# Performance work log

Hardware: AMD Instinct MI355X
Metric: run time of the kernel (lower is better)

Reference implementation:

```python
import jax, jax.numpy as jnp
import numpy as np

N0 = 50000
N1 = 50000
E = 500000
IN_DIM = 128
OUT_DIM = 128
H = 8
DK = OUT_DIM // H  # 16
SQRT_DK = float(np.sqrt(DK))
NUM_TYPES = 2
NUM_REL = 3
# relations: (src_type, dst_type, e_id)
RELATIONS = [(0, 1, 0), (1, 0, 1), (0, 0, 2)]


def setup_inputs() -> dict:
    key = jax.random.key(0)
    ks = jax.random.split(key, 24)
    d = {}
    d["h0"] = jax.random.normal(ks[0], (N0, IN_DIM), dtype=jnp.float32)
    d["h1"] = jax.random.normal(ks[1], (N1, IN_DIM), dtype=jnp.float32)
    d["src0"] = jax.random.randint(ks[2], (E,), 0, N0)
    d["dst0"] = jax.random.randint(ks[3], (E,), 0, N1)
    d["src1"] = jax.random.randint(ks[4], (E,), 0, N1)
    d["dst1"] = jax.random.randint(ks[5], (E,), 0, N0)
    d["src2"] = jax.random.randint(ks[6], (E,), 0, N0)
    d["dst2"] = jax.random.randint(ks[7], (E,), 0, N0)
    w_scale = 1.0 / np.sqrt(IN_DIM)
    # per-node-type stacked linear weights (k, q, v, a), torch Linear convention: y = x @ W.T + b
    d["Wk"] = jax.random.normal(ks[8], (NUM_TYPES, OUT_DIM, IN_DIM), dtype=jnp.float32) * w_scale
    d["bk"] = jnp.zeros((NUM_TYPES, OUT_DIM), dtype=jnp.float32)
    d["Wq"] = jax.random.normal(ks[9], (NUM_TYPES, OUT_DIM, IN_DIM), dtype=jnp.float32) * w_scale
    d["bq"] = jnp.zeros((NUM_TYPES, OUT_DIM), dtype=jnp.float32)
    d["Wv"] = jax.random.normal(ks[10], (NUM_TYPES, OUT_DIM, IN_DIM), dtype=jnp.float32) * w_scale
    d["bv"] = jnp.zeros((NUM_TYPES, OUT_DIM), dtype=jnp.float32)
    d["Wa"] = jax.random.normal(ks[11], (NUM_TYPES, OUT_DIM, OUT_DIM), dtype=jnp.float32) * w_scale
    d["ba"] = jnp.zeros((NUM_TYPES, OUT_DIM), dtype=jnp.float32)
    xavier = float(np.sqrt(6.0 / (DK + DK)))
    d["rel_att"] = jax.random.uniform(ks[12], (NUM_REL, H, DK, DK), dtype=jnp.float32, minval=-xavier, maxval=xavier)
    d["rel_msg"] = jax.random.uniform(ks[13], (NUM_REL, H, DK, DK), dtype=jnp.float32, minval=-xavier, maxval=xavier)
    d["rel_pri"] = jnp.ones((NUM_REL, H), dtype=jnp.float32)
    d["skip"] = jnp.ones((NUM_TYPES,), dtype=jnp.float32)
    return d


def _lin(x, W, b):
    return x @ W.T + b


def reference(h0, h1, src0, dst0, src1, dst1, src2, dst2,
              Wk, bk, Wq, bq, Wv, bv, Wa, ba,
              rel_att, rel_msg, rel_pri, skip):
    h = [h0, h1]
    edges = [(src0, dst0), (src1, dst1), (src2, dst2)]
    # per-type projections, reshaped to (N, H, DK)
    k = [_lin(h[t], Wk[t], bk[t]).reshape(-1, H, DK) for t in range(NUM_TYPES)]
    q = [_lin(h[t], Wq[t], bq[t]).reshape(-1, H, DK) for t in range(NUM_TYPES)]
    v = [_lin(h[t], Wv[t], bv[t]).reshape(-1, H, DK) for t in range(NUM_TYPES)]

    agg = [[] for _ in range(NUM_TYPES)]
    for (s, dt, e), (src, dst) in zip(RELATIONS, edges):
        # relation-specific transforms of source k and v
        kr = jnp.einsum('nhi,hij->nhj', k[s], rel_att[e])
        vr = jnp.einsum('nhi,hij->nhj', v[s], rel_msg[e])
        # per-edge dot-product score (E, H)
        score = (q[dt][dst] * kr[src]).sum(-1) * rel_pri[e] / SQRT_DK
        n_dst = h[dt].shape[0]
        # edge softmax normalized by dst (stable)
        m = jax.ops.segment_max(score, dst, num_segments=n_dst)
        ex = jnp.exp(score - m[dst])
        den = jax.ops.segment_sum(ex, dst, num_segments=n_dst)
        attn = ex / den[dst]  # (E, H)
        # weighted message scatter-sum -> (n_dst, H, DK)
        msg = vr[src] * attn[:, :, None]
        agg[dt].append(jax.ops.segment_sum(msg, dst, num_segments=n_dst))

    new_h = []
    for t in range(NUM_TYPES):
        # cross_reducer='mean' over relations targeting this node type
        tmean = sum(agg[t]) / float(len(agg[t]))
        tflat = tmean.reshape(-1, OUT_DIM)
        trans = _lin(tflat, Wa[t], ba[t])  # dropout = identity (eval)
        alpha = jax.nn.sigmoid(skip[t])
        new_h.append(trans * alpha + h[t] * (1.0 - alpha))
    return tuple(new_h)
```

## Files before the change

### kernel.cpp

```cpp
#include <hip/hip_runtime.h>

typedef __attribute__((ext_vector_type(8))) short bf16x8;
typedef __attribute__((ext_vector_type(4))) float f32x4;

#define NB 196
#define CHK 2048
#define CAPB 4096

__device__ __forceinline__ float bflo(unsigned u) { return __uint_as_float(u << 16); }
__device__ __forceinline__ float bfhi(unsigned u) { return __uint_as_float(u & 0xFFFF0000u); }
__device__ __forceinline__ unsigned f2bf(float f) {
  unsigned u = __float_as_uint(f);
  u = (u + 0x7FFFu + ((u >> 16) & 1u)) >> 16;
  return u;
}

__global__ void cvt2_kernel(const float* __restrict__ a, unsigned short* __restrict__ oa,
                            const float* __restrict__ b, unsigned short* __restrict__ ob,
                            int n8) {
  int i = blockIdx.x * 256 + threadIdx.x;
  if (i >= n8) return;
  const float* in = blockIdx.y ? b : a;
  unsigned short* out = blockIdx.y ? ob : oa;
  const float4* p = (const float4*)(in + (size_t)i * 8);
  float4 x = p[0], y = p[1];
  uint4 v;
  v.x = f2bf(x.x) | (f2bf(x.y) << 16);
  v.y = f2bf(x.z) | (f2bf(x.w) << 16);
  v.z = f2bf(y.x) | (f2bf(y.y) << 16);
  v.w = f2bf(y.z) | (f2bf(y.w) << 16);
  *(uint4*)(out + (size_t)i * 8) = v;
}

__global__ void compose_w_kernel(const float* __restrict__ Wk, const float* __restrict__ bk,
                                 const float* __restrict__ Wv, const float* __restrict__ bv,
                                 const float* __restrict__ rel_att, const float* __restrict__ rel_msg,
                                 const float* __restrict__ rel_pri,
                                 unsigned short* __restrict__ Wkr, float* __restrict__ bkr,
                                 unsigned short* __restrict__ Wvr, float* __restrict__ bvr) {
  int e = blockIdx.x;
  int o = blockIdx.y;
  int z = blockIdx.z;
  int c = threadIdx.x;
  int hd = o >> 4, j = o & 15;
  const int se[3] = {0, 1, 0};
  int s = se[e];
  const float* W = z ? Wv : Wk;
  const float* b = z ? bv : bk;
  const float* R = z ? rel_msg : rel_att;
  float scale = z ? 1.0f : (rel_pri[e * 8 + hd] * 0.25f);
  float acc = 0.0f, bacc = 0.0f;
#pragma unroll
  for (int i = 0; i < 16; ++i) {
    float r = R[((e * 8 + hd) * 16 + i) * 16 + j];
    acc += W[(s * 128 + hd * 16 + i) * 128 + c] * r;
    bacc += b[s * 128 + hd * 16 + i] * r;
  }
  unsigned short* Wo = z ? Wvr : Wkr;
  float* bo = z ? bvr : bkr;
  Wo[((size_t)e * 128 + o) * 128 + c] = (unsigned short)f2bf(acc * scale);
  if (c == 0) bo[e * 128 + o] = bacc * scale;
}

struct ProjFP {
  const float* A[2];
  int M[2];
  int nj[2];
  const unsigned short* W[10];
  const float* b[10];
  unsigned short* out[10];
  int ostr[10];
};

__global__ __launch_bounds__(256) void proj_gemm_fused(ProjFP P) {
  __shared__ short As[128 * 128];
  __shared__ short Bs[128 * 128];
  int type = blockIdx.y;
  const float* __restrict__ A = P.A[type];
  int M = P.M[type];
  int nj = P.nj[type];
  int base = type * 5;
  int row0 = blockIdx.x * 128;
  if (row0 >= M) return;
  int t = threadIdx.x;
  bool full = (row0 + 128 <= M);
#pragma unroll
  for (int it = 0; it < 8; ++it) {
    int o = (it * 256 + t) * 8;
    int row = o >> 7, col = o & 127;
    int gr = row0 + row;
    uint4 av = make_uint4(0, 0, 0, 0);
    if (full || gr < M) {
      float4 x = *(const float4*)(A + (size_t)gr * 128 + col);
      float4 y = *(const float4*)(A + (size_t)gr * 128 + col + 4);
      av.x = f2bf(x.x) | (f2bf(x.y) << 16);
      av.y = f2bf(x.z) | (f2bf(x.w) << 16);
      av.z = f2bf(y.x) | (f2bf(y.y) << 16);
      av.w = f2bf(y.z) | (f2bf(y.w) << 16);
    }
    int sw = o ^ ((row & 7) << 3);
    *(uint4*)(&As[sw]) = av;
  }
  {
    const unsigned short* W0 = P.W[base];
#pragma unroll
    for (int it = 0; it < 8; ++it) {
      int o = (it * 256 + t) * 8;
      int row = o >> 7;
      int sw = o ^ ((row & 7) << 3);
      *(uint4*)(&Bs[sw]) = *(const uint4*)(W0 + o);
    }
  }
  __syncthreads();
  int wid = t >> 6, l = t & 63;
  int wr = wid >> 1, wc = wid & 1;
  int lr = l & 15, kb = l >> 4;
  for (int j = 0;; ++j) {
    f32x4 acc[4][4] = {};
#pragma unroll
    for (int ks = 0; ks < 4; ++ks) {
      bf16x8 af[4], bfr[4];
#pragma unroll
      for (int m = 0; m < 4; ++m) {
        int row = wr * 64 + m * 16 + lr;
        int h = (row * 128 + kb * 8 + ks * 32) ^ ((row & 7) << 3);
        af[m] = *(bf16x8*)(&As[h]);
      }
#pragma unroll
      for (int n = 0; n < 4; ++n) {
        int row = wc * 64 + n * 16 + lr;
        int h = (row * 128 + kb * 8 + ks * 32) ^ ((row & 7) << 3);
        bfr[n] = *(bf16x8*)(&Bs[h]);
      }
#pragma unroll
      for (int m = 0; m < 4; ++m)
#pragma unroll
        for (int n = 0; n < 4; ++n)
          acc[m][n] = __builtin_amdgcn_mfma_f32_16x16x32_bf16(af[m], bfr[n], acc[m][n], 0, 0, 0);
    }
    const float* bias = P.b[base + j];
    unsigned short* out = P.out[base + j];
    int ostr = P.ostr[base + j];
    int rb = row0 + wr * 64 + (l >> 4) * 4;
#pragma unroll
    for (int m = 0; m < 4; ++m)
#pragma unroll
      for (int jr = 0; jr < 4; ++jr) {
        int grow = rb + m * 16 + jr;
        if (grow < M) {
#pragma unroll
          for (int n = 0; n < 4; ++n) {
            int col = wc * 64 + n * 16 + lr;
            out[(size_t)grow * ostr + col] = (unsigned short)f2bf(acc[m][n][jr] + bias[col]);
          }
        }
      }
    if (j + 1 >= nj) break;
    __syncthreads();
    {
      const unsigned short* Wj = P.W[base + j + 1];
#pragma unroll
      for (int it = 0; it < 8; ++it) {
        int o = (it * 256 + t) * 8;
        int row = o >> 7;
        int sw = o ^ ((row & 7) << 3);
        *(uint4*)(&Bs[sw]) = *(const uint4*)(Wj + o);
      }
    }
    __syncthreads();
  }
}

__global__ __launch_bounds__(256) void final_gemm_mfma(
    float* __restrict__ dout, const unsigned short* __restrict__ Tb0,
    const unsigned short* __restrict__ Tb1, const unsigned short* __restrict__ Wab,
    const float* __restrict__ ba, const float* __restrict__ h0, const float* __restrict__ h1,
    const float* __restrict__ skip, int N0, int N1) {
  __shared__ short As[128 * 128];
  __shared__ short Bs[128 * 128];
  int type = blockIdx.y;
  int M = type ? N1 : N0;
  const unsigned short* T = type ? Tb1 : Tb0;
  const unsigned short* W = Wab + (size_t)type * 16384;
  const float* bias = ba + type * 128;
  const float* h = type ? h1 : h0;
  float* O = dout + (type ? (size_t)N0 * 128 : 0);
  int row0 = blockIdx.x * 128;
  if (row0 >= M) return;
  int t = threadIdx.x;
  bool full = (row0 + 128 <= M);
#pragma unroll
  for (int it = 0; it < 8; ++it) {
    int o = (it * 256 + t) * 8;
    int row = o >> 7;
    int gr = row0 + row;
    uint4 av = make_uint4(0, 0, 0, 0);
    if (full || gr < M) av = *(const uint4*)(T + (size_t)gr * 128 + (o & 127));
    int sw = o ^ ((row & 7) << 3);
    *(uint4*)(&As[sw]) = av;
    uint4 wv = *(const uint4*)(W + o);
    *(uint4*)(&Bs[sw]) = wv;
  }
  __syncthreads();
  int wid = t >> 6, l = t & 63;
  int wr = wid >> 1, wc = wid & 1;
  int lr = l & 15, kb = l >> 4;
  f32x4 acc[4][4] = {};
#pragma unroll
  for (int ks = 0; ks < 4; ++ks) {
    bf16x8 af[4], bfr[4];
#pragma unroll
    for (int m = 0; m < 4; ++m) {
      int row = wr * 64 + m * 16 + lr;
      int h2 = (row * 128 + kb * 8 + ks * 32) ^ ((row & 7) << 3);
      af[m] = *(bf16x8*)(&As[h2]);
    }
#pragma unroll
    for (int n = 0; n < 4; ++n) {
      int row = wc * 64 + n * 16 + lr;
      int h2 = (row * 128 + kb * 8 + ks * 32) ^ ((row & 7) << 3);
      bfr[n] = *(bf16x8*)(&Bs[h2]);
    }
#pragma unroll
    for (int m = 0; m < 4; ++m)
#pragma unroll
      for (int n = 0; n < 4; ++n)
        acc[m][n] = __builtin_amdgcn_mfma_f32_16x16x32_bf16(af[m], bfr[n], acc[m][n], 0, 0, 0);
  }
  float alpha = 1.0f / (1.0f + __expf(-skip[type]));
  float beta = 1.0f - alpha;
  int rb = row0 + wr * 64 + (l >> 4) * 4;
#pragma unroll
  for (int m = 0; m < 4; ++m)
#pragma unroll
    for (int jr = 0; jr < 4; ++jr) {
      int grow = rb + m * 16 + jr;
      if (grow < M) {
#pragma unroll
        for (int n = 0; n < 4; ++n) {
          int col = wc * 64 + n * 16 + lr;
          float vout = alpha * (acc[m][n][jr] + bias[col]) + beta * h[(size_t)grow * 128 + col];
          O[(size_t)grow * 128 + col] = vout;
        }
      }
    }
}


__global__ __launch_bounds__(256) void bhist_kernel(const int* __restrict__ d0,
                                                    const int* __restrict__ d1,
                                                    const int* __restrict__ d2,
                                                    int* __restrict__ bh, int E) {
  __shared__ int lh[NB];
  int r = blockIdx.y;
  const int* dst = r == 0 ? d0 : (r == 1 ? d1 : d2);
  int t = threadIdx.x;
  int lo = blockIdx.x * CHK;
  int hi = lo + CHK < E ? lo + CHK : E;
  for (int j = t; j < NB; j += 256) lh[j] = 0;
  __syncthreads();
  for (int i = lo + t; i < hi; i += 256) atomicAdd(&lh[dst[i] >> 8], 1);
  __syncthreads();
  for (int j = t; j < NB; j += 256) {
    int v = lh[j];
    if (v) atomicAdd(&bh[r * NB + j], v);
  }
}

__global__ void bscan_kernel(const int* __restrict__ bh, int* __restrict__ bbase, int E) {
  __shared__ int sdm[256];
  int r = blockIdx.x;
  int t = threadIdx.x;
  int v = (t < NB) ? bh[r * NB + t] : 0;
  sdm[t] = v;
  __syncthreads();
  for (int off = 1; off < 256; off <<= 1) {
    int u = (t >= off) ? sdm[t - off] : 0;
    __syncthreads();
    sdm[t] += u;
    __syncthreads();
  }
  if (t < NB) bbase[r * (NB + 1) + t] = sdm[t] - v;
  if (t == 0) bbase[r * (NB + 1) + NB] = E;
}

__global__ __launch_bounds__(256) void bin_kernel(
    const int* __restrict__ s0, const int* __restrict__ d0, const int* __restrict__ s1,
    const int* __restrict__ d1, const int* __restrict__ s2, const int* __restrict__ d2,
    const int* __restrict__ bbase, int* __restrict__ bcur, int2* __restrict__ bo0,
    int2* __restrict__ bo1, int2* __restrict__ bo2, int E) {
  __shared__ int2 st[CHK];
  __shared__ int ga[CHK];
  __shared__ int hist[NB];
  __shared__ int scn[256];
  __shared__ int gb[NB];
  int r = blockIdx.y;
  const int* src = r == 0 ? s0 : (r == 1 ? s1 : s2);
  const int* dst = r == 0 ? d0 : (r == 1 ? d1 : d2);
  int2* bo = r == 0 ? bo0 : (r == 1 ? bo1 : bo2);
  const int* bb = bbase + r * (NB + 1);
  int t = threadIdx.x;
  int lo = blockIdx.x * CHK;
  int hi = lo + CHK < E ? lo + CHK : E;
  int nloc = hi - lo;
  if (nloc <= 0) return;
  for (int j = t; j < NB; j += 256) hist[j] = 0;
  __syncthreads();
  int myb[CHK / 256], myr[CHK / 256];
  int2 mye[CHK / 256];
#pragma unroll
  for (int k = 0; k < CHK / 256; ++k) {
    int i = lo + k * 256 + t;
    myb[k] = -1;
    if (i < hi) {
      int d = dst[i];
      int b = d >> 8;
      mye[k] = make_int2(src[i], d);
      myb[k] = b;
      myr[k] = atomicAdd(&hist[b], 1);
    }
  }
  __syncthreads();
  int v = (t < NB) ? hist[t] : 0;
  scn[t] = v;
  __syncthreads();
  for (int off = 1; off < 256; off <<= 1) {
    int u = (t >= off) ? scn[t - off] : 0;
    __syncthreads();
    scn[t] += u;
    __syncthreads();
  }
  int excl = scn[t] - v;
  __syncthreads();
  scn[t] = excl;
  if (t < NB && v > 0) gb[t] = atomicAdd(&bcur[r * NB + t], v);
  __syncthreads();
#pragma unroll
  for (int k = 0; k < CHK / 256; ++k) {
    if (myb[k] >= 0) {
      int slot = scn[myb[k]] + myr[k];
      st[slot] = mye[k];
      ga[slot] = bb[myb[k]] + gb[myb[k]] + myr[k];
    }
  }
  __syncthreads();
  for (int j = t; j < nloc; j += 256) bo[ga[j]] = st[j];
}

__global__ __launch_bounds__(256) void bsort_kernel(
    const int2* __restrict__ bo0, const int2* __restrict__ bo1, const int2* __restrict__ bo2,
    const int* __restrict__ bbase, int* __restrict__ rp0, int* __restrict__ rp1,
    int* __restrict__ rp2, int* __restrict__ ss0, int* __restrict__ ss1, int* __restrict__ ss2,
    int* __restrict__ dof0, int* __restrict__ dof1, int* __restrict__ dof2, int nd0, int nd1,
    int nd2, int E) {
  __shared__ int2 ed[CAPB];
  __shared__ int ssrt[CAPB];
  __shared__ unsigned short rank[CAPB];
  __shared__ unsigned short dsrtu[CAPB];
  __shared__ int hist[256];
  __shared__ int scn[256];
  int r = blockIdx.y, b = blockIdx.x;
  const int2* bo = r == 0 ? bo0 : (r == 1 ? bo1 : bo2);
  int* rp = r == 0 ? rp0 : (r == 1 ? rp1 : rp2);
  int* ss = r == 0 ? ss0 : (r == 1 ? ss1 : ss2);
  int* dof = r == 0 ? dof0 : (r == 1 ? dof1 : dof2);
  int nd = r == 0 ? nd0 : (r == 1 ? nd1 : nd2);
  const int* bb = bbase + r * (NB + 1);
  int base = bb[b], endb = bb[b + 1];
  int cnt = endb - base;
  if (cnt > CAPB) cnt = CAPB;
  int nlo = b << 8;
  int nn = nd - nlo;
  if (nn > 256) nn = 256;
  int t = threadIdx.x;
  hist[t] = 0;
  for (int j = t; j < cnt; j += 256) ed[j] = bo[base + j];
  __syncthreads();
  for (int j = t; j < cnt; j += 256) {
    int node = ed[j].y & 255;
    rank[j] = (unsigned short)atomicAdd(&hist[node], 1);
  }
  __syncthreads();
  int v = hist[t];
  scn[t] = v;
  __syncthreads();
  for (int off = 1; off < 256; off <<= 1) {
    int u = (t >= off) ? scn[t - off] : 0;
    __syncthreads();
    scn[t] += u;
    __syncthreads();
  }
  int excl = scn[t] - v;
  __syncthreads();
  scn[t] = excl;
  __syncthreads();
  if (t < nn) rp[nlo + t] = base + excl;
  if (b == 0 && t == 0) rp[nd] = E;
  for (int j = t; j < cnt; j += 256) {
    int node = ed[j].y & 255;
    int slot = scn[node] + rank[j];
    ssrt[slot] = ed[j].x;
    dsrtu[slot] = (unsigned short)node;
  }
  __syncthreads();
  for (int j = t; j < cnt; j += 256) {
    ss[base + j] = ssrt[j];
    dof[base + j] = nlo + dsrtu[j];
  }
}

struct ScP {
  const int* ss[3];
  const int* dof[3];
  const unsigned* kv[3];
  const unsigned* qb[3];
  unsigned short* eb[3];
  int E;
};

__global__ __launch_bounds__(256) void score_kernel(ScP P) {
  int r = blockIdx.y;
  const int* __restrict__ ss = P.ss[r];
  const int* __restrict__ dof = P.dof[r];
  const unsigned* __restrict__ kv = P.kv[r];
  const unsigned* __restrict__ qb = P.qb[r];
  unsigned short* __restrict__ eb = P.eb[r];
  int t = threadIdx.x;
  int p = blockIdx.x * 32 + (t >> 3);
  if (p >= P.E) return;
  int h = t & 7;
  int s = ss[p];
  int d = dof[p];
  const uint4* kr = (const uint4*)((const char*)kv + ((size_t)(unsigned)s << 9) + h * 32);
  const uint4* qr = (const uint4*)((const char*)qb + ((size_t)(unsigned)d << 8) + h * 32);
  uint4 k1 = kr[0], k2 = kr[1];
  uint4 q1 = qr[0], q2 = qr[1];
  float sc = 0.f;
#pragma unroll
  for (int c = 0; c < 4; ++c) {
    unsigned ku = ((const unsigned*)&k1)[c], qu = ((const unsigned*)&q1)[c];
    sc = fmaf(bflo(ku), bflo(qu), sc);
    sc = fmaf(bfhi(ku), bfhi(qu), sc);
  }
#pragma unroll
  for (int c = 0; c < 4; ++c) {
    unsigned ku = ((const unsigned*)&k2)[c], qu = ((const unsigned*)&q2)[c];
    sc = fmaf(bflo(ku), bflo(qu), sc);
    sc = fmaf(bfhi(ku), bfhi(qu), sc);
  }
  eb[(size_t)p * 8 + h] = (unsigned short)f2bf(__expf(sc));
}

struct AgP {
  const int *ss0, *ss1, *ss2;
  const unsigned short *eb0, *eb1, *eb2;
  const unsigned *kv0, *kv1, *kv2;
  const int *rp0, *rp1, *rp2;
  unsigned *Tb0, *Tb1;
  int N0, N1;
};

__device__ __forceinline__ void agg_rel(const int* __restrict__ ss,
                                        const unsigned short* __restrict__ eb,
                                        const unsigned* __restrict__ kv,
                                        const int* __restrict__ rp, int node, int l,
                                        float& r0, float& r1) {
  int beg = __builtin_amdgcn_readfirstlane(rp[node]);
  int end = __builtin_amdgcn_readfirstlane(rp[node + 1]);
  if (end <= beg) return;
  int h = l >> 3;
  const char* kvl = (const char*)kv + 256 + l * 4;
  float a0 = 0.f, a1 = 0.f, den = 0.f;
  for (int p = beg; p < end; p += 4) {
    int idx = p + (l & 3);
    idx = idx < end ? idx : end - 1;
    int sv = ss[idx];
#pragma unroll
    for (int j = 0; j < 4; ++j) {
      int pj = p + j;
      bool valid = pj < end;
      int pj2 = valid ? pj : end - 1;
      int s = __builtin_amdgcn_readlane(sv, j);
      float e = __uint_as_float((unsigned)eb[(size_t)pj2 * 8 + h] << 16);
      if (j && !valid) e = 0.f;
      unsigned v = *(const unsigned*)(kvl + ((size_t)(unsigned)s << 9));
      den += e;
      a0 = fmaf(e, bflo(v), a0);
      a1 = fmaf(e, bfhi(v), a1);
    }
  }
  float inv = 1.0f / den;
  r0 = fmaf(a0, inv, r0);
  r1 = fmaf(a1, inv, r1);
}

__global__ __launch_bounds__(256) void agg2_kernel(AgP P) {
  int gw = (blockIdx.x * 256 + threadIdx.x) >> 6;
  int l = threadIdx.x & 63;
  if (gw < P.N0) {
    float r0 = 0.f, r1 = 0.f;
    agg_rel(P.ss1, P.eb1, P.kv1, P.rp1, gw, l, r0, r1);
    agg_rel(P.ss2, P.eb2, P.kv2, P.rp2, gw, l, r0, r1);
    P.Tb0[(size_t)gw * 64 + l] = f2bf(r0 * 0.5f) | (f2bf(r1 * 0.5f) << 16);
  } else if (gw < P.N0 + P.N1) {
    int n = gw - P.N0;
    float r0 = 0.f, r1 = 0.f;
    agg_rel(P.ss0, P.eb0, P.kv0, P.rp0, n, l, r0, r1);
    P.Tb1[(size_t)n * 64 + l] = f2bf(r0) | (f2bf(r1) << 16);
  }
}

extern "C" void kernel_launch(void* const* d_in, const int* in_sizes, int n_in,
                              void* d_out, int out_size, void* d_ws, size_t ws_size,
                              hipStream_t stream) {
  const float* h0 = (const float*)d_in[0];
  const float* h1 = (const float*)d_in[1];
  const int* srcs[3] = {(const int*)d_in[2], (const int*)d_in[4], (const int*)d_in[6]};
  const int* dsts[3] = {(const int*)d_in[3], (const int*)d_in[5], (const int*)d_in[7]};
  const float* Wk = (const float*)d_in[8];
  const float* bk = (const float*)d_in[9];
  const float* Wq = (const float*)d_in[10];
  const float* bq = (const float*)d_in[11];
  const float* Wv = (const float*)d_in[12];
  const float* bv = (const float*)d_in[13];
  const float* Wa = (const float*)d_in[14];
  const float* ba = (const float*)d_in[15];
  const float* rel_att = (const float*)d_in[16];
  const float* rel_msg = (const float*)d_in[17];
  const float* rel_pri = (const float*)d_in[18];
  const float* skip = (const float*)d_in[19];

  int N0 = in_sizes[0] / 128;
  int N1 = in_sizes[1] / 128;
  int E = in_sizes[2];
  int nsrc[3] = {N0, N1, N0};
  int ndst[3] = {N1, N0, N0};
  int maxN = N0 > N1 ? N0 : N1;

  char* base = (char*)d_ws;
  size_t off = 0;
  auto alloc = [&](size_t bytes) -> void* {
    void* p = base + off;
    off += (bytes + 255) & ~(size_t)255;
    return p;
  };

  unsigned short* qb0 = (unsigned short*)alloc((size_t)N0 * 128 * 2);
  unsigned short* qb1 = (unsigned short*)alloc((size_t)N1 * 128 * 2);
  unsigned short* kvb[3];
  for (int r = 0; r < 3; ++r) kvb[r] = (unsigned short*)alloc((size_t)nsrc[r] * 256 * 2);
  unsigned short* Tb0 = (unsigned short*)alloc((size_t)N0 * 128 * 2);
  unsigned short* Tb1 = (unsigned short*)alloc((size_t)N1 * 128 * 2);
  unsigned short* Wkrb = (unsigned short*)alloc((size_t)3 * 16384 * 2);
  unsigned short* Wvrb = (unsigned short*)alloc((size_t)3 * 16384 * 2);
  unsigned short* Wqb = (unsigned short*)alloc((size_t)2 * 16384 * 2);
  unsigned short* Wab = (unsigned short*)alloc((size_t)2 * 16384 * 2);
  float* bkr = (float*)alloc(3 * 128 * 4);
  float* bvr = (float*)alloc(3 * 128 * 4);
  int* rp[3];
  int* ssb[3];
  int* dof[3];
  unsigned short* eb[3];
  int2* bo[3];
  for (int r = 0; r < 3; ++r) {
    rp[r] = (int*)alloc((size_t)(ndst[r] + 1) * 4);
    ssb[r] = (int*)alloc((size_t)(E + 8) * 4);
    dof[r] = (int*)alloc((size_t)(E + 8) * 4);
    eb[r] = (unsigned short*)alloc((size_t)E * 8 * 2);
    bo[r] = (int2*)alloc((size_t)(E + 8) * 8);
  }
  int* bcnt = (int*)alloc((size_t)2 * 3 * NB * 4);
  int* bhist = bcnt;
  int* bcur = bcnt + 3 * NB;
  int* bbase = (int*)alloc((size_t)3 * (NB + 1) * 4);
  (void)ws_size;

  compose_w_kernel<<<dim3(3, 128, 2), 128, 0, stream>>>(Wk, bk, Wv, bv, rel_att, rel_msg,
                                                        rel_pri, Wkrb, bkr, Wvrb, bvr);
  cvt2_kernel<<<dim3(16, 2), 256, 0, stream>>>(Wq, Wqb, Wa, Wab, 4096);

  ProjFP pf;
  pf.A[0] = h0; pf.A[1] = h1;
  pf.M[0] = N0; pf.M[1] = N1;
  pf.nj[0] = 5; pf.nj[1] = 3;
  pf.W[0] = Wqb;            pf.b[0] = bq;        pf.out[0] = qb0;          pf.ostr[0] = 128;
  pf.W[1] = Wkrb;           pf.b[1] = bkr;       pf.out[1] = kvb[0];       pf.ostr[1] = 256;
  pf.W[2] = Wkrb + 32768;   pf.b[2] = bkr + 256; pf.out[2] = kvb[2];       pf.ostr[2] = 256;
  pf.W[3] = Wvrb;           pf.b[3] = bvr;       pf.out[3] = kvb[0] + 128; pf.ostr[3] = 256;
  pf.W[4] = Wvrb + 32768;   pf.b[4] = bvr + 256; pf.out[4] = kvb[2] + 128; pf.ostr[4] = 256;
  pf.W[5] = Wqb + 16384;    pf.b[5] = bq + 128;  pf.out[5] = qb1;          pf.ostr[5] = 128;
  pf.W[6] = Wkrb + 16384;   pf.b[6] = bkr + 128; pf.out[6] = kvb[1];       pf.ostr[6] = 256;
  pf.W[7] = Wvrb + 16384;   pf.b[7] = bvr + 128; pf.out[7] = kvb[1] + 128; pf.ostr[7] = 256;
  pf.W[8] = Wqb; pf.b[8] = bq; pf.out[8] = qb0; pf.ostr[8] = 128;
  pf.W[9] = Wqb; pf.b[9] = bq; pf.out[9] = qb0; pf.ostr[9] = 128;
  proj_gemm_fused<<<dim3((maxN + 127) / 128, 2), 256, 0, stream>>>(pf);

  hipMemsetAsync(bcnt, 0, (size_t)2 * 3 * NB * 4, stream);
  bhist_kernel<<<dim3((E + CHK - 1) / CHK, 3), 256, 0, stream>>>(dsts[0], dsts[1], dsts[2],
                                                                 bhist, E);
  bscan_kernel<<<3, 256, 0, stream>>>(bhist, bbase, E);
  bin_kernel<<<dim3((E + CHK - 1) / CHK, 3), 256, 0, stream>>>(
      srcs[0], dsts[0], srcs[1], dsts[1], srcs[2], dsts[2], bbase, bcur, bo[0], bo[1], bo[2], E);
  bsort_kernel<<<dim3(NB, 3), 256, 0, stream>>>(
      bo[0], bo[1], bo[2], bbase, rp[0], rp[1], rp[2], ssb[0], ssb[1], ssb[2], dof[0], dof[1],
      dof[2], ndst[0], ndst[1], ndst[2], E);

  ScP sp;
  for (int r = 0; r < 3; ++r) {
    sp.ss[r] = ssb[r];
    sp.dof[r] = dof[r];
    sp.kv[r] = (const unsigned*)kvb[r];
    sp.eb[r] = eb[r];
  }
  sp.qb[0] = (const unsigned*)qb1;
  sp.qb[1] = (const unsigned*)qb0;
  sp.qb[2] = (const unsigned*)qb0;
  sp.E = E;
  score_kernel<<<dim3((E + 31) / 32, 3), 256, 0, stream>>>(sp);

  AgP ap;
  ap.ss0 = ssb[0]; ap.ss1 = ssb[1]; ap.ss2 = ssb[2];
  ap.eb0 = eb[0]; ap.eb1 = eb[1]; ap.eb2 = eb[2];
  ap.kv0 = (const unsigned*)kvb[0]; ap.kv1 = (const unsigned*)kvb[1];
  ap.kv2 = (const unsigned*)kvb[2];
  ap.rp0 = rp[0]; ap.rp1 = rp[1]; ap.rp2 = rp[2];
  ap.Tb0 = (unsigned*)Tb0; ap.Tb1 = (unsigned*)Tb1;
  ap.N0 = N0; ap.N1 = N1;
  int totw = N0 + N1;
  agg2_kernel<<<(totw + 3) / 4, 256, 0, stream>>>(ap);

  final_gemm_mfma<<<dim3((maxN + 127) / 128, 2), 256, 0, stream>>>(
      (float*)d_out, Tb0, Tb1, Wab, ba, h0, h1, skip, N0, N1);
}
```

Measured before the change: 263.6 us.

## Pack src/dst into 16-bit pairs and double-buffer V gathers in aggregation

Edge source and destination indices are packed into a single 32-bit word (16 bits each) through binning, bucket sort, score and aggregation. This halves index traffic and drops the separate dof array. The aggregation kernel is also restructured: each wave splits into two halves that each handle 4 edges of an 8-edge group, with 8-byte V loads per lane, software double-buffered prefetch, and a final cross-half shuffle reduction. The packing relies on node counts fitting in 16 bits (50000 < 65536), so it breaks for larger graphs.

```diff
diff --git a/kernel.cpp b/kernel.cpp
--- a/kernel.cpp
+++ b/kernel.cpp
@@ -287,9 +287,9 @@
 __global__ __launch_bounds__(256) void bin_kernel(
     const int* __restrict__ s0, const int* __restrict__ d0, const int* __restrict__ s1,
     const int* __restrict__ d1, const int* __restrict__ s2, const int* __restrict__ d2,
-    const int* __restrict__ bbase, int* __restrict__ bcur, int2* __restrict__ bo0,
-    int2* __restrict__ bo1, int2* __restrict__ bo2, int E) {
-  __shared__ int2 st[CHK];
+    const int* __restrict__ bbase, int* __restrict__ bcur, unsigned* __restrict__ bo0,
+    unsigned* __restrict__ bo1, unsigned* __restrict__ bo2, int E) {
+  __shared__ unsigned st[CHK];
   __shared__ int ga[CHK];
   __shared__ int hist[NB];
   __shared__ int scn[256];
@@ -297,7 +297,7 @@
   int r = blockIdx.y;
   const int* src = r == 0 ? s0 : (r == 1 ? s1 : s2);
   const int* dst = r == 0 ? d0 : (r == 1 ? d1 : d2);
-  int2* bo = r == 0 ? bo0 : (r == 1 ? bo1 : bo2);
+  unsigned* bo = r == 0 ? bo0 : (r == 1 ? bo1 : bo2);
   const int* bb = bbase + r * (NB + 1);
   int t = threadIdx.x;
   int lo = blockIdx.x * CHK;
@@ -307,7 +307,7 @@
   for (int j = t; j < NB; j += 256) hist[j] = 0;
   __syncthreads();
   int myb[CHK / 256], myr[CHK / 256];
-  int2 mye[CHK / 256];
+  unsigned mye[CHK / 256];
 #pragma unroll
   for (int k = 0; k < CHK / 256; ++k) {
     int i = lo + k * 256 + t;
@@ -315,7 +315,7 @@
     if (i < hi) {
       int d = dst[i];
       int b = d >> 8;
-      mye[k] = make_int2(src[i], d);
+      mye[k] = (unsigned)src[i] | ((unsigned)d << 16);
       myb[k] = b;
       myr[k] = atomicAdd(&hist[b], 1);
     }
@@ -348,22 +348,19 @@
 }
 
 __global__ __launch_bounds__(256) void bsort_kernel(
-    const int2* __restrict__ bo0, const int2* __restrict__ bo1, const int2* __restrict__ bo2,
-    const int* __restrict__ bbase, int* __restrict__ rp0, int* __restrict__ rp1,
-    int* __restrict__ rp2, int* __restrict__ ss0, int* __restrict__ ss1, int* __restrict__ ss2,
-    int* __restrict__ dof0, int* __restrict__ dof1, int* __restrict__ dof2, int nd0, int nd1,
-    int nd2, int E) {
-  __shared__ int2 ed[CAPB];
-  __shared__ int ssrt[CAPB];
+    const unsigned* __restrict__ bo0, const unsigned* __restrict__ bo1,
+    const unsigned* __restrict__ bo2, const int* __restrict__ bbase, int* __restrict__ rp0,
+    int* __restrict__ rp1, int* __restrict__ rp2, unsigned* __restrict__ sp0,
+    unsigned* __restrict__ sp1, unsigned* __restrict__ sp2, int nd0, int nd1, int nd2, int E) {
+  __shared__ unsigned ed[CAPB];
+  __shared__ unsigned srt[CAPB];
   __shared__ unsigned short rank[CAPB];
-  __shared__ unsigned short dsrtu[CAPB];
   __shared__ int hist[256];
   __shared__ int scn[256];
   int r = blockIdx.y, b = blockIdx.x;
-  const int2* bo = r == 0 ? bo0 : (r == 1 ? bo1 : bo2);
+  const unsigned* bo = r == 0 ? bo0 : (r == 1 ? bo1 : bo2);
   int* rp = r == 0 ? rp0 : (r == 1 ? rp1 : rp2);
-  int* ss = r == 0 ? ss0 : (r == 1 ? ss1 : ss2);
-  int* dof = r == 0 ? dof0 : (r == 1 ? dof1 : dof2);
+  unsigned* sp = r == 0 ? sp0 : (r == 1 ? sp1 : sp2);
   int nd = r == 0 ? nd0 : (r == 1 ? nd1 : nd2);
   const int* bb = bbase + r * (NB + 1);
   int base = bb[b], endb = bb[b + 1];
@@ -377,7 +374,7 @@
   for (int j = t; j < cnt; j += 256) ed[j] = bo[base + j];
   __syncthreads();
   for (int j = t; j < cnt; j += 256) {
-    int node = ed[j].y & 255;
+    int node = (ed[j] >> 16) & 255;
     rank[j] = (unsigned short)atomicAdd(&hist[node], 1);
   }
   __syncthreads();
@@ -397,21 +394,15 @@
   if (t < nn) rp[nlo + t] = base + excl;
   if (b == 0 && t == 0) rp[nd] = E;
   for (int j = t; j < cnt; j += 256) {
-    int node = ed[j].y & 255;
-    int slot = scn[node] + rank[j];
-    ssrt[slot] = ed[j].x;
-    dsrtu[slot] = (unsigned short)node;
-  }
-  __syncthreads();
-  for (int j = t; j < cnt; j += 256) {
-    ss[base + j] = ssrt[j];
-    dof[base + j] = nlo + dsrtu[j];
-  }
+    int node = (ed[j] >> 16) & 255;
+    srt[scn[node] + rank[j]] = ed[j];
+  }
+  __syncthreads();
+  for (int j = t; j < cnt; j += 256) sp[base + j] = srt[j];
 }
 
 struct ScP {
-  const int* ss[3];
-  const int* dof[3];
+  const unsigned* sp[3];
   const unsigned* kv[3];
   const unsigned* qb[3];
   unsigned short* eb[3];
@@ -420,8 +411,7 @@
 
 __global__ __launch_bounds__(256) void score_kernel(ScP P) {
   int r = blockIdx.y;
-  const int* __restrict__ ss = P.ss[r];
-  const int* __restrict__ dof = P.dof[r];
+  const unsigned* __restrict__ sp = P.sp[r];
   const unsigned* __restrict__ kv = P.kv[r];
   const unsigned* __restrict__ qb = P.qb[r];
   unsigned short* __restrict__ eb = P.eb[r];
@@ -429,10 +419,11 @@
   int p = blockIdx.x * 32 + (t >> 3);
   if (p >= P.E) return;
   int h = t & 7;
-  int s = ss[p];
-  int d = dof[p];
-  const uint4* kr = (const uint4*)((const char*)kv + ((size_t)(unsigned)s << 9) + h * 32);
-  const uint4* qr = (const uint4*)((const char*)qb + ((size_t)(unsigned)d << 8) + h * 32);
+  unsigned pk = sp[p];
+  unsigned s = pk & 0xFFFFu;
+  unsigned d = pk >> 16;
+  const uint4* kr = (const uint4*)((const char*)kv + ((size_t)s << 9) + h * 32);
+  const uint4* qr = (const uint4*)((const char*)qb + ((size_t)d << 8) + h * 32);
   uint4 k1 = kr[0], k2 = kr[1];
   uint4 q1 = qr[0], q2 = qr[1];
   float sc = 0.f;
@@ -452,7 +443,7 @@
 }
 
 struct AgP {
-  const int *ss0, *ss1, *ss2;
+  const unsigned *sp0, *sp1, *sp2;
   const unsigned short *eb0, *eb1, *eb2;
   const unsigned *kv0, *kv1, *kv2;
   const int *rp0, *rp1, *rp2;
@@ -460,53 +451,100 @@
   int N0, N1;
 };
 
-__device__ __forceinline__ void agg_rel(const int* __restrict__ ss,
+__device__ __forceinline__ void loadV(const char* __restrict__ kvl,
+                                      const unsigned* __restrict__ sp, int p, int lastp,
+                                      int half, uint2 vb[4]) {
+  int idx = p + (threadIdx.x & 7);
+  idx = idx > lastp ? lastp : idx;
+  unsigned sv = sp[idx];
+#pragma unroll
+  for (int g = 0; g < 4; ++g) {
+    unsigned plo = __builtin_amdgcn_readlane(sv, g);
+    unsigned phi = __builtin_amdgcn_readlane(sv, g + 4);
+    unsigned pk = half ? phi : plo;
+    vb[g] = *(const uint2*)(kvl + ((size_t)(pk & 0xFFFFu) << 9));
+  }
+}
+
+__device__ __forceinline__ void computeV(const unsigned short* __restrict__ eb, int p, int end,
+                                         int lastp, int half, int h, const uint2 vb[4],
+                                         float& a0, float& a1, float& a2, float& a3,
+                                         float& den) {
+#pragma unroll
+  for (int g = 0; g < 4; ++g) {
+    int pj = p + (half << 2) + g;
+    int pj2 = pj > lastp ? lastp : pj;
+    float e = __uint_as_float((unsigned)eb[(size_t)pj2 * 8 + h] << 16);
+    e *= (pj < end) ? 1.f : 0.f;
+    den += e;
+    a0 = fmaf(e, bflo(vb[g].x), a0);
+    a1 = fmaf(e, bfhi(vb[g].x), a1);
+    a2 = fmaf(e, bflo(vb[g].y), a2);
+    a3 = fmaf(e, bfhi(vb[g].y), a3);
+  }
+}
+
+__device__ __forceinline__ void agg_rel(const unsigned* __restrict__ sp,
                                         const unsigned short* __restrict__ eb,
                                         const unsigned* __restrict__ kv,
-                                        const int* __restrict__ rp, int node, int l,
-                                        float& r0, float& r1) {
+                                        const int* __restrict__ rp, int node, int ll, int half,
+                                        float& r0, float& r1, float& r2, float& r3) {
   int beg = __builtin_amdgcn_readfirstlane(rp[node]);
   int end = __builtin_amdgcn_readfirstlane(rp[node + 1]);
   if (end <= beg) return;
-  int h = l >> 3;
-  const char* kvl = (const char*)kv + 256 + l * 4;
-  float a0 = 0.f, a1 = 0.f, den = 0.f;
-  for (int p = beg; p < end; p += 4) {
-    int idx = p + (l & 3);
-    idx = idx < end ? idx : end - 1;
-    int sv = ss[idx];
-#pragma unroll
-    for (int j = 0; j < 4; ++j) {
-      int pj = p + j;
-      bool valid = pj < end;
-      int pj2 = valid ? pj : end - 1;
-      int s = __builtin_amdgcn_readlane(sv, j);
-      float e = __uint_as_float((unsigned)eb[(size_t)pj2 * 8 + h] << 16);
-      if (j && !valid) e = 0.f;
-      unsigned v = *(const unsigned*)(kvl + ((size_t)(unsigned)s << 9));
-      den += e;
-      a0 = fmaf(e, bflo(v), a0);
-      a1 = fmaf(e, bfhi(v), a1);
-    }
-  }
+  int lastp = end - 1;
+  int h = ll >> 2;
+  const char* kvl = (const char*)kv + 256 + ll * 8;
+  float a0 = 0.f, a1 = 0.f, a2 = 0.f, a3 = 0.f, den = 0.f;
+  uint2 va[4], vb[4];
+  int p = beg;
+  loadV(kvl, sp, p, lastp, half, va);
+  for (;;) {
+    if (p + 8 < end) loadV(kvl, sp, p + 8, lastp, half, vb);
+    computeV(eb, p, end, lastp, half, h, va, a0, a1, a2, a3, den);
+    p += 8;
+    if (p >= end) break;
+    if (p + 8 < end) loadV(kvl, sp, p + 8, lastp, half, va);
+    computeV(eb, p, end, lastp, half, h, vb, a0, a1, a2, a3, den);
+    p += 8;
+    if (p >= end) break;
+  }
+  den += __shfl_xor(den, 32);
+  a0 += __shfl_xor(a0, 32);
+  a1 += __shfl_xor(a1, 32);
+  a2 += __shfl_xor(a2, 32);
+  a3 += __shfl_xor(a3, 32);
   float inv = 1.0f / den;
   r0 = fmaf(a0, inv, r0);
   r1 = fmaf(a1, inv, r1);
+  r2 = fmaf(a2, inv, r2);
+  r3 = fmaf(a3, inv, r3);
 }
 
 __global__ __launch_bounds__(256) void agg2_kernel(AgP P) {
   int gw = (blockIdx.x * 256 + threadIdx.x) >> 6;
   int l = threadIdx.x & 63;
+  int ll = l & 31, half = l >> 5;
   if (gw < P.N0) {
-    float r0 = 0.f, r1 = 0.f;
-    agg_rel(P.ss1, P.eb1, P.kv1, P.rp1, gw, l, r0, r1);
-    agg_rel(P.ss2, P.eb2, P.kv2, P.rp2, gw, l, r0, r1);
-    P.Tb0[(size_t)gw * 64 + l] = f2bf(r0 * 0.5f) | (f2bf(r1 * 0.5f) << 16);
+    float r0 = 0.f, r1 = 0.f, r2 = 0.f, r3 = 0.f;
+    agg_rel(P.sp1, P.eb1, P.kv1, P.rp1, gw, ll, half, r0, r1, r2, r3);
+    agg_rel(P.sp2, P.eb2, P.kv2, P.rp2, gw, ll, half, r0, r1, r2, r3);
+    if (half == 0) {
+      uint2 o;
+      o.x = f2bf(r0 * 0.5f) | (f2bf(r1 * 0.5f) << 16);
+      o.y = f2bf(r2 * 0.5f) | (f2bf(r3 * 0.5f) << 16);
+      *(uint2*)(P.Tb0 + (size_t)gw * 64 + 2 * ll) = o;
+    }
   } else if (gw < P.N0 + P.N1) {
     int n = gw - P.N0;
-    float r0 = 0.f, r1 = 0.f;
-    agg_rel(P.ss0, P.eb0, P.kv0, P.rp0, n, l, r0, r1);
-    P.Tb1[(size_t)n * 64 + l] = f2bf(r0) | (f2bf(r1) << 16);
+    float r0 = 0.f, r1 = 0.f, r2 = 0.f, r3 = 0.f;
+    agg_rel(P.sp0, P.eb0, P.kv0, P.rp0, n, ll, half, r0, r1, r2, r3);
+    if (half == 0) {
+      uint2 o;
+      o.x = f2bf(r0) | (f2bf(r1) << 16);
+      o.y = f2bf(r2) | (f2bf(r3) << 16);
+      *(uint2*)(P.Tb1 + (size_t)n * 64 + 2 * ll) = o;
+    }
   }
 }
 
@@ -558,16 +596,14 @@
   float* bkr = (float*)alloc(3 * 128 * 4);
   float* bvr = (float*)alloc(3 * 128 * 4);
   int* rp[3];
-  int* ssb[3];
-  int* dof[3];
+  unsigned* spk[3];
   unsigned short* eb[3];
-  int2* bo[3];
+  unsigned* bo[3];
   for (int r = 0; r < 3; ++r) {
     rp[r] = (int*)alloc((size_t)(ndst[r] + 1) * 4);
-    ssb[r] = (int*)alloc((size_t)(E + 8) * 4);
-    dof[r] = (int*)alloc((size_t)(E + 8) * 4);
+    spk[r] = (unsigned*)alloc((size_t)(E + 8) * 4);
     eb[r] = (unsigned short*)alloc((size_t)E * 8 * 2);
-    bo[r] = (int2*)alloc((size_t)(E + 8) * 8);
+    bo[r] = (unsigned*)alloc((size_t)(E + 8) * 4);
   }
   int* bcnt = (int*)alloc((size_t)2 * 3 * NB * 4);
   int* bhist = bcnt;
@@ -602,13 +638,12 @@
   bin_kernel<<<dim3((E + CHK - 1) / CHK, 3), 256, 0, stream>>>(
       srcs[0], dsts[0], srcs[1], dsts[1], srcs[2], dsts[2], bbase, bcur, bo[0], bo[1], bo[2], E);
   bsort_kernel<<<dim3(NB, 3), 256, 0, stream>>>(
-      bo[0], bo[1], bo[2], bbase, rp[0], rp[1], rp[2], ssb[0], ssb[1], ssb[2], dof[0], dof[1],
-      dof[2], ndst[0], ndst[1], ndst[2], E);
+      bo[0], bo[1], bo[2], bbase, rp[0], rp[1], rp[2], spk[0], spk[1], spk[2], ndst[0],
+      ndst[1], ndst[2], E);
 
   ScP sp;
   for (int r = 0; r < 3; ++r) {
-    sp.ss[r] = ssb[r];
-    sp.dof[r] = dof[r];
+    sp.sp[r] = spk[r];
     sp.kv[r] = (const unsigned*)kvb[r];
     sp.eb[r] = eb[r];
   }
@@ -619,7 +654,7 @@
   score_kernel<<<dim3((E + 31) / 32, 3), 256, 0, stream>>>(sp);
 
   AgP ap;
-  ap.ss0 = ssb[0]; ap.ss1 = ssb[1]; ap.ss2 = ssb[2];
+  ap.sp0 = spk[0]; ap.sp1 = spk[1]; ap.sp2 = spk[2];
   ap.eb0 = eb[0]; ap.eb1 = eb[1]; ap.eb2 = eb[2];
   ap.kv0 = (const unsigned*)kvb[0]; ap.kv1 = (const unsigned*)kvb[1];
   ap.kv2 = (const unsigned*)kvb[2];
```

Measured after the change: 250.0 us. -5.2%, faster.
